# Kernel optimization log

Measured on AMD Instinct MI355X. Metric: run time of the kernel, lower is better.

## Reference

```python
import jax, jax.numpy as jnp
import numpy as np

EPS = 1e-09
TOP_K = 2


def setup_inputs() -> dict:
    key = jax.random.key(0)
    k1, k2 = jax.random.split(key)
    N, D, E = 32768, 1024, 64
    x = jax.random.normal(k1, (N, D), dtype=jnp.float32)
    gate_w = jax.random.normal(k2, (E, D), dtype=jnp.float32) * (1.0 / np.sqrt(D))
    return {"x": x, "gate_w": gate_w}


def reference(x, gate_w):
    # logits: [N, E] = x @ gate_w.T  (nn.Linear with no bias)
    logits = jnp.einsum("nd,ed->ne", x, gate_w)
    probs = jax.nn.softmax(logits, axis=-1)
    # aux load-balancing loss (stored on buffer in torch; returned here)
    mean_probs = probs.mean(axis=0)  # [E]
    aux_loss = jnp.sum(mean_probs * jnp.log(mean_probs + EPS))
    # top-k selection + renormalize
    top_k_weights, top_k_indices = jax.lax.top_k(probs, TOP_K)  # [N, K]
    top_k_weights = top_k_weights / (top_k_weights.sum(axis=-1, keepdims=True) + EPS)
    return top_k_weights, top_k_indices, aux_loss
```

## Files before the change

### kernel.cpp

```cpp
#include <hip/hip_runtime.h>
#include <hip/hip_bf16.h>
#include <math.h>

#define NROWS 32768
#define DDIM  1024
#define NEXP  64
#define TAU   2e-4f
#define EPSF  1e-9f
#define CAPMAX 8192
#define NSHARD 8
#define NCH   16

typedef __attribute__((ext_vector_type(8)))  short  short8;
typedef __attribute__((ext_vector_type(16))) float  f32x16;
typedef __attribute__((address_space(3))) unsigned int       lds_u32;
typedef __attribute__((address_space(1))) const unsigned int g_u32;

__device__ __forceinline__ bool gt_(float a, int ea, float b, int eb)
{ return a > b || (a == b && ea < eb); }

__device__ __forceinline__ void cvt_hl(float f, short& h, short& l)
{
    __hip_bfloat16 hb = __float2bfloat16(f);
    float r = f - __bfloat162float(hb);
    __hip_bfloat16 lb = __float2bfloat16(r);
    h = *reinterpret_cast<short*>(&hb);
    l = *reinterpret_cast<short*>(&lb);
}

__global__ void wpack_kernel(const float* __restrict__ gw,
                             unsigned short* __restrict__ wp,
                             float* __restrict__ shard,
                             int* __restrict__ cnt)
{
    if (blockIdx.x == 0) {
        shard[threadIdx.x]       = 0.0f;
        shard[256 + threadIdx.x] = 0.0f;
        if (threadIdx.x == 0) *cnt = 0;
    }
    const int kc = blockIdx.x;
    const int t  = threadIdx.x;
    const int lane = t & 63, g = (t >> 6) & 1, pr = t >> 7;
    const int e = g * 32 + (lane & 31);
    const int k = kc * 16 + (lane >> 5) * 8;
    float4 f0 = *reinterpret_cast<const float4*>(gw + (size_t)e * DDIM + k);
    float4 f1 = *reinterpret_cast<const float4*>(gw + (size_t)e * DDIM + k + 4);
    float f[8] = {f0.x, f0.y, f0.z, f0.w, f1.x, f1.y, f1.z, f1.w};
    short8 o;
    #pragma unroll
    for (int j = 0; j < 8; ++j) {
        short hh, ll;
        cvt_hl(f[j], hh, ll);
        o[j] = pr ? ll : hh;
    }
    *reinterpret_cast<short8*>(wp + ((size_t)((kc * 2 + g) * 2 + pr) * 64 + lane) * 8) = o;
}

__global__ __launch_bounds__(128, 2) void moe_main(
    const float* __restrict__ x, const unsigned short* __restrict__ wp,
    float* __restrict__ out, float* __restrict__ shard,
    int* __restrict__ cnt, int* __restrict__ list, int cap)
{
    extern __shared__ char smem[];

    const int t = threadIdx.x;
    const int g = t >> 6;
    const int lane = t & 63;
    const int l31 = lane & 31, l5 = lane >> 5;
    const int row0 = blockIdx.x * 32;
    const int arow = l31;
    const int xr   = (arow & 7) << 4;

    f32x16 acc;
    #pragma unroll
    for (int r = 0; r < 16; ++r) acc[r] = 0.0f;

    int srow[4], scol[4];
    #pragma unroll
    for (int q = 0; q < 4; ++q) {
        int d = q * 2048 + t * 16;
        srow[q] = d >> 8;
        scol[q] = (d & 255) ^ ((srow[q] & 7) << 4);
    }

    const char* wqb = (const char*)wp + (size_t)g * 2048 + (size_t)lane * 16;

    #define STAGE(c_) do {                                                       \
        const char* xs0_ = (const char*)x + (size_t)row0 * 4096 + (size_t)(c_) * 256; \
        const int xb_ = ((c_) & 3) * 8192;                                       \
        _Pragma("unroll")                                                        \
        for (int q_ = 0; q_ < 4; ++q_) {                                         \
            int d_ = q_ * 2048 + t * 16;                                         \
            const char* xsrc_ = xs0_ + (size_t)srow[q_] * 4096 + scol[q_];       \
            __builtin_amdgcn_global_load_lds((g_u32*)xsrc_,                      \
                (lds_u32*)(smem + xb_ + d_), 16, 0, 0);                          \
        }                                                                        \
    } while (0)

    #define BLOAD(dst_, c_) do {                                                 \
        _Pragma("unroll")                                                        \
        for (int kcl_ = 0; kcl_ < 4; ++kcl_) {                                   \
            const char* b_ = wqb + (size_t)((c_) * 4 + kcl_) * 4096;             \
            dst_[kcl_][0] = *reinterpret_cast<const short8*>(b_);                \
            dst_[kcl_][1] = *reinterpret_cast<const short8*>(b_ + 1024);         \
        }                                                                        \
    } while (0)

    short8 Bc[4][2], Bn[4][2];

    STAGE(0); STAGE(1); STAGE(2);
    BLOAD(Bc, 0);

    for (int i = 0; i < NCH; ++i) {
        if (i < NCH - 1) BLOAD(Bn, i + 1);
        if (i < NCH - 3) STAGE(i + 3);
        __builtin_amdgcn_sched_barrier(0);
        if (i == 0)               { asm volatile("s_waitcnt vmcnt(12)" ::: "memory"); }
        else if (i < NCH - 3)     { asm volatile("s_waitcnt vmcnt(16)" ::: "memory"); }
        else if (i == NCH - 3)    { asm volatile("s_waitcnt vmcnt(12)" ::: "memory"); }
        else if (i == NCH - 2)    { asm volatile("s_waitcnt vmcnt(8)" ::: "memory"); }
        else                      { asm volatile("s_waitcnt vmcnt(0)" ::: "memory"); }
        __builtin_amdgcn_s_barrier();
        __builtin_amdgcn_sched_barrier(0);

        const int xb = (i & 3) * 8192;
        const char* xrow = smem + xb + arow * 256;
        #pragma unroll
        for (int kcl = 0; kcl < 4; ++kcl) {
            const int cb = kcl * 64 + l5 * 32;
            float4 f0 = *reinterpret_cast<const float4*>(xrow + (cb ^ xr));
            float4 f1 = *reinterpret_cast<const float4*>(xrow + ((cb + 16) ^ xr));
            float f[8] = {f0.x, f0.y, f0.z, f0.w, f1.x, f1.y, f1.z, f1.w};
            short8 ah, al;
            #pragma unroll
            for (int jj = 0; jj < 8; ++jj) {
                short hh, ll;
                cvt_hl(f[jj], hh, ll);
                ah[jj] = hh; al[jj] = ll;
            }
            acc = __builtin_amdgcn_mfma_f32_32x32x16_bf16(ah, Bc[kcl][0], acc, 0, 0, 0);
            acc = __builtin_amdgcn_mfma_f32_32x32x16_bf16(al, Bc[kcl][0], acc, 0, 0, 0);
            acc = __builtin_amdgcn_mfma_f32_32x32x16_bf16(ah, Bc[kcl][1], acc, 0, 0, 0);
        }
        #pragma unroll
        for (int kcl = 0; kcl < 4; ++kcl) {
            Bc[kcl][0] = Bn[kcl][0];
            Bc[kcl][1] = Bn[kcl][1];
        }
        __builtin_amdgcn_sched_barrier(0);
        __builtin_amdgcn_s_barrier();
        __builtin_amdgcn_sched_barrier(0);
    }
    #undef STAGE
    #undef BLOAD

    float* lgs = reinterpret_cast<float*>(smem);
    __syncthreads();
    #pragma unroll
    for (int r = 0; r < 16; ++r) {
        const int lrow = (r & 3) + 8 * (r >> 2) + 4 * l5;
        lgs[lrow * 68 + g * 32 + l31] = acc[r];
    }
    __syncthreads();

    const int erow = t >> 2, q = t & 3;
    float L[16];
    #pragma unroll
    for (int i = 0; i < 4; ++i) {
        float4 v = *reinterpret_cast<const float4*>(lgs + erow * 68 + q * 16 + i * 4);
        L[4*i] = v.x; L[4*i+1] = v.y; L[4*i+2] = v.z; L[4*i+3] = v.w;
    }
    float v1 = -3.4e38f, v2 = -3.4e38f, v3 = -3.4e38f;
    int   e1 = 1 << 30,  e2 = 1 << 30,  e3 = 1 << 30;
    #pragma unroll
    for (int i = 0; i < 16; ++i) {
        float v = L[i]; int e = q * 16 + i;
        if      (gt_(v, e, v1, e1)) { v3=v2; e3=e2; v2=v1; e2=e1; v1=v; e1=e; }
        else if (gt_(v, e, v2, e2)) { v3=v2; e3=e2; v2=v; e2=e; }
        else if (gt_(v, e, v3, e3)) { v3=v; e3=e; }
    }
    #pragma unroll
    for (int m = 1; m <= 2; m <<= 1) {
        float o1 = __shfl_xor(v1, m), o2 = __shfl_xor(v2, m), o3 = __shfl_xor(v3, m);
        int  oe1 = __shfl_xor(e1, m), oe2 = __shfl_xor(e2, m), oe3 = __shfl_xor(e3, m);
        float n1, n2, n3; int m1, m2, m3;
        if (gt_(v1, e1, o1, oe1)) {
            n1 = v1; m1 = e1;
            if (gt_(v2, e2, o1, oe1)) {
                n2 = v2; m2 = e2;
                if (gt_(v3, e3, o1, oe1)) { n3 = v3; m3 = e3; } else { n3 = o1; m3 = oe1; }
            } else {
                n2 = o1; m2 = oe1;
                if (gt_(v2, e2, o2, oe2)) { n3 = v2; m3 = e2; } else { n3 = o2; m3 = oe2; }
            }
        } else {
            n1 = o1; m1 = oe1;
            if (gt_(o2, oe2, v1, e1)) {
                n2 = o2; m2 = oe2;
                if (gt_(o3, oe3, v1, e1)) { n3 = o3; m3 = oe3; } else { n3 = v1; m3 = e1; }
            } else {
                n2 = v1; m2 = e1;
                if (gt_(o2, oe2, v2, e2)) { n3 = o2; m3 = oe2; } else { n3 = v2; m3 = e2; }
            }
        }
        v1 = n1; e1 = m1; v2 = n2; e2 = m2; v3 = n3; e3 = m3;
    }
    float pr[16], sl = 0.0f;
    #pragma unroll
    for (int i = 0; i < 16; ++i) { pr[i] = expf(L[i] - v1); sl += pr[i]; }
    float S = sl;
    S += __shfl_xor(S, 1); S += __shfl_xor(S, 2);
    const float invS = 1.0f / S;
    #pragma unroll
    for (int i = 0; i < 16; ++i) pr[i] *= invS;
    #pragma unroll
    for (int m = 4; m <= 32; m <<= 1)
        #pragma unroll
        for (int i = 0; i < 16; ++i) pr[i] += __shfl_xor(pr[i], m);
    float* auxred = lgs + 32 * 68;
    if (lane < 4) {
        #pragma unroll
        for (int i = 0; i < 16; ++i) auxred[g * 64 + q * 16 + i] = pr[i];
    }
    if (q == 0) {
        const float p1 = invS;
        const float p2 = expf(v2 - v1) * invS;
        const float dn = p1 + p2 + EPSF;
        const int r = row0 + erow;
        out[2 * r]                 = p1 / dn;
        out[2 * r + 1]             = p2 / dn;
        out[2 * NROWS + 2 * r]     = (float)e1;
        out[2 * NROWS + 2 * r + 1] = (float)e2;
        if (cap > 0 && (v1 - v2 < TAU || v2 - v3 < TAU)) {
            int pos = atomicAdd(cnt, 1);
            if (pos < cap) list[pos] = r;
        }
    }
    __syncthreads();
    if (t < 64) {
        float s = auxred[t] + auxred[64 + t];
        atomicAdd(&shard[(blockIdx.x & (NSHARD - 1)) * 64 + t], s);
    }
}

__global__ __launch_bounds__(256) void finalize_kernel(
    const float* __restrict__ x, const float* __restrict__ gw,
    float* __restrict__ out, const float* __restrict__ shard,
    const int* __restrict__ cnt, const int* __restrict__ list, int cap)
{
    if (blockIdx.x == 0) {
        const int tt = threadIdx.x;
        if (tt < 64) {
            float m = 0.0f;
            #pragma unroll
            for (int s = 0; s < NSHARD; ++s) m += shard[s * 64 + tt];
            m *= (1.0f / (float)NROWS);
            float v = m * logf(m + EPSF);
            #pragma unroll
            for (int k = 1; k <= 32; k <<= 1) v += __shfl_xor(v, k);
            if (tt == 0) out[4 * NROWS] = v;
        }
        return;
    }
    __shared__ float lg[64];
    const int n = (cap > 0) ? min(*cnt, cap) : 0;
    const int tt = threadIdx.x, e = tt >> 2, part = tt & 3;
    for (int j = (int)blockIdx.x - 1; j < n; j += 64) {
        const int row = list[j];
        const float* xrp = x  + (size_t)row * DDIM + part * 256;
        const float* wrp = gw + (size_t)e   * DDIM + part * 256;
        float a = 0.0f;
        #pragma unroll 8
        for (int kk = 0; kk < 64; ++kk) {
            float4 xv = *reinterpret_cast<const float4*>(xrp + kk * 4);
            float4 wv = *reinterpret_cast<const float4*>(wrp + kk * 4);
            a += xv.x * wv.x + xv.y * wv.y + xv.z * wv.z + xv.w * wv.w;
        }
        a += __shfl_xor(a, 1); a += __shfl_xor(a, 2);
        if (part == 0) lg[e] = a;
        __syncthreads();
        if (tt < 4) {
            const int q = tt;
            float v1 = -3.4e38f, v2 = -3.4e38f; int e1 = 1 << 30, e2 = 1 << 30;
            float Lr[16];
            #pragma unroll
            for (int i = 0; i < 16; ++i) {
                float v = Lr[i] = lg[q * 16 + i]; int ee = q * 16 + i;
                if      (gt_(v, ee, v1, e1)) { v2 = v1; e2 = e1; v1 = v; e1 = ee; }
                else if (gt_(v, ee, v2, e2)) { v2 = v; e2 = ee; }
            }
            #pragma unroll
            for (int m = 1; m <= 2; m <<= 1) {
                float o1 = __shfl_xor(v1, m), o2 = __shfl_xor(v2, m);
                int  oe1 = __shfl_xor(e1, m), oe2 = __shfl_xor(e2, m);
                float n1, n2; int m1, m2;
                if (gt_(v1, e1, o1, oe1)) {
                    n1 = v1; m1 = e1;
                    if (gt_(v2, e2, o1, oe1)) { n2 = v2; m2 = e2; } else { n2 = o1; m2 = oe1; }
                } else {
                    n1 = o1; m1 = oe1;
                    if (gt_(o2, oe2, v1, e1)) { n2 = o2; m2 = oe2; } else { n2 = v1; m2 = e1; }
                }
                v1 = n1; e1 = m1; v2 = n2; e2 = m2;
            }
            float s = 0.0f;
            #pragma unroll
            for (int i = 0; i < 16; ++i) s += expf(Lr[i] - v1);
            s += __shfl_xor(s, 1); s += __shfl_xor(s, 2);
            if (q == 0) {
                const float invS = 1.0f / s;
                const float p1 = invS, p2 = expf(v2 - v1) * invS;
                const float dn = p1 + p2 + EPSF;
                out[2 * row]                 = p1 / dn;
                out[2 * row + 1]             = p2 / dn;
                out[2 * NROWS + 2 * row]     = (float)e1;
                out[2 * NROWS + 2 * row + 1] = (float)e2;
            }
        }
        __syncthreads();
    }
}

extern "C" void kernel_launch(void* const* d_in, const int* in_sizes, int n_in,
                              void* d_out, int out_size, void* d_ws, size_t ws_size,
                              hipStream_t stream)
{
    const float* x  = (const float*)d_in[0];
    const float* gw = (const float*)d_in[1];
    float* out      = (float*)d_out;

    unsigned short* wp = (unsigned short*)d_ws;
    float* shard   = (float*)((char*)d_ws + 262144);
    int*   cnt     = (int*)((char*)d_ws + 264192);
    int*   list    = (int*)((char*)d_ws + 264448);
    int cap = 0;
    if (ws_size >= 264448 + 4096) {
        size_t avail = (ws_size - 264448) / sizeof(int);
        cap = (avail > CAPMAX) ? CAPMAX : (int)avail;
    }

    hipLaunchKernelGGL(wpack_kernel, dim3(64), dim3(256), 0, stream,
                       gw, wp, shard, cnt);
    hipLaunchKernelGGL(moe_main, dim3(NROWS / 32), dim3(128), 32768, stream,
                       x, wp, out, shard, cnt, list, cap);
    hipLaunchKernelGGL(finalize_kernel, dim3(65), dim3(256), 0, stream,
                       x, gw, out, shard, cnt, list, cap);
}
```

Baseline: 61.36 us.

## Fuse ambiguous-row fp32 recompute and aux-loss finalize into main kernel

Removes the separate finalize kernel. Each block now marks near-tie rows in a shared bitmask and recomputes their logits in exact fp32 in place, and the last block to finish, found through an atomic done counter, reduces the shard sums into the aux loss. This saves a kernel launch and the global list/counter traffic. The cost is a serialized per-row recompute inside blocks that have ambiguous rows, with extra syncs, and the tie threshold is halved to cut how many rows need it. The smaller threshold may let rows whose bf16-split top-k differs from fp32 go uncorrected.

```diff
diff --git a/kernel.cpp b/kernel.cpp
--- a/kernel.cpp
+++ b/kernel.cpp
@@ -5,11 +5,11 @@
 #define NROWS 32768
 #define DDIM  1024
 #define NEXP  64
-#define TAU   2e-4f
+#define TAU   1e-4f
 #define EPSF  1e-9f
-#define CAPMAX 8192
 #define NSHARD 8
 #define NCH   16
+#define NBLK  1024
 
 typedef __attribute__((ext_vector_type(8)))  short  short8;
 typedef __attribute__((ext_vector_type(16))) float  f32x16;
@@ -31,12 +31,12 @@
 __global__ void wpack_kernel(const float* __restrict__ gw,
                              unsigned short* __restrict__ wp,
                              float* __restrict__ shard,
-                             int* __restrict__ cnt)
+                             int* __restrict__ done)
 {
     if (blockIdx.x == 0) {
         shard[threadIdx.x]       = 0.0f;
         shard[256 + threadIdx.x] = 0.0f;
-        if (threadIdx.x == 0) *cnt = 0;
+        if (threadIdx.x == 0) *done = 0;
     }
     const int kc = blockIdx.x;
     const int t  = threadIdx.x;
@@ -57,11 +57,12 @@
 }
 
 __global__ __launch_bounds__(128, 2) void moe_main(
-    const float* __restrict__ x, const unsigned short* __restrict__ wp,
-    float* __restrict__ out, float* __restrict__ shard,
-    int* __restrict__ cnt, int* __restrict__ list, int cap)
+    const float* __restrict__ x, const float* __restrict__ gw,
+    const unsigned short* __restrict__ wp, float* __restrict__ out,
+    float* __restrict__ shard, int* __restrict__ done)
 {
     extern __shared__ char smem[];
+    __shared__ unsigned ambig;
 
     const int t = threadIdx.x;
     const int g = t >> 6;
@@ -70,6 +71,8 @@
     const int row0 = blockIdx.x * 32;
     const int arow = l31;
     const int xr   = (arow & 7) << 4;
+
+    if (t == 0) ambig = 0u;
 
     f32x16 acc;
     #pragma unroll
@@ -231,93 +234,95 @@
         out[2 * r + 1]             = p2 / dn;
         out[2 * NROWS + 2 * r]     = (float)e1;
         out[2 * NROWS + 2 * r + 1] = (float)e2;
-        if (cap > 0 && (v1 - v2 < TAU || v2 - v3 < TAU)) {
-            int pos = atomicAdd(cnt, 1);
-            if (pos < cap) list[pos] = r;
-        }
+        if (v1 - v2 < TAU || v2 - v3 < TAU)
+            atomicOr(&ambig, 1u << erow);
     }
     __syncthreads();
     if (t < 64) {
         float s = auxred[t] + auxred[64 + t];
         atomicAdd(&shard[(blockIdx.x & (NSHARD - 1)) * 64 + t], s);
     }
-}
-
-__global__ __launch_bounds__(256) void finalize_kernel(
-    const float* __restrict__ x, const float* __restrict__ gw,
-    float* __restrict__ out, const float* __restrict__ shard,
-    const int* __restrict__ cnt, const int* __restrict__ list, int cap)
-{
-    if (blockIdx.x == 0) {
-        const int tt = threadIdx.x;
-        if (tt < 64) {
+
+    unsigned am = ambig;
+    if (am) {
+        float* lg = lgs;
+        const int re = t >> 1, part = t & 1;
+        while (am) {
+            const int rloc = __ffs((int)am) - 1;
+            am &= am - 1;
+            const int row = row0 + rloc;
+            const float* xrp = x  + (size_t)row * DDIM + part * 512;
+            const float* wrp = gw + (size_t)re  * DDIM + part * 512;
+            float a = 0.0f;
+            #pragma unroll 8
+            for (int kk = 0; kk < 128; ++kk) {
+                float4 xv = *reinterpret_cast<const float4*>(xrp + kk * 4);
+                float4 wv = *reinterpret_cast<const float4*>(wrp + kk * 4);
+                a += xv.x * wv.x + xv.y * wv.y + xv.z * wv.z + xv.w * wv.w;
+            }
+            a += __shfl_xor(a, 1);
+            __syncthreads();
+            if (part == 0) lg[re] = a;
+            __syncthreads();
+            if (t < 4) {
+                const int qq = t;
+                float w1 = -3.4e38f, w2 = -3.4e38f; int f1i = 1 << 30, f2i = 1 << 30;
+                float Lr[16];
+                #pragma unroll
+                for (int i = 0; i < 16; ++i) {
+                    float v = Lr[i] = lg[qq * 16 + i]; int ee = qq * 16 + i;
+                    if      (gt_(v, ee, w1, f1i)) { w2 = w1; f2i = f1i; w1 = v; f1i = ee; }
+                    else if (gt_(v, ee, w2, f2i)) { w2 = v; f2i = ee; }
+                }
+                #pragma unroll
+                for (int m = 1; m <= 2; m <<= 1) {
+                    float o1 = __shfl_xor(w1, m), o2 = __shfl_xor(w2, m);
+                    int  oe1 = __shfl_xor(f1i, m), oe2 = __shfl_xor(f2i, m);
+                    float n1, n2; int m1, m2;
+                    if (gt_(w1, f1i, o1, oe1)) {
+                        n1 = w1; m1 = f1i;
+                        if (gt_(w2, f2i, o1, oe1)) { n2 = w2; m2 = f2i; } else { n2 = o1; m2 = oe1; }
+                    } else {
+                        n1 = o1; m1 = oe1;
+                        if (gt_(o2, oe2, w1, f1i)) { n2 = o2; m2 = oe2; } else { n2 = w1; m2 = f1i; }
+                    }
+                    w1 = n1; f1i = m1; w2 = n2; f2i = m2;
+                }
+                float s = 0.0f;
+                #pragma unroll
+                for (int i = 0; i < 16; ++i) s += expf(Lr[i] - w1);
+                s += __shfl_xor(s, 1); s += __shfl_xor(s, 2);
+                if (qq == 0) {
+                    const float is = 1.0f / s;
+                    const float p1 = is, p2 = expf(w2 - w1) * is;
+                    const float dn = p1 + p2 + EPSF;
+                    out[2 * row]                 = p1 / dn;
+                    out[2 * row + 1]             = p2 / dn;
+                    out[2 * NROWS + 2 * row]     = (float)f1i;
+                    out[2 * NROWS + 2 * row + 1] = (float)f2i;
+                }
+            }
+            __syncthreads();
+        }
+    }
+
+    __syncthreads();
+    __threadfence();
+    __shared__ int rank;
+    if (t == 0) rank = atomicAdd(done, 1);
+    __syncthreads();
+    if (rank == NBLK - 1) {
+        __threadfence();
+        if (t < 64) {
             float m = 0.0f;
             #pragma unroll
-            for (int s = 0; s < NSHARD; ++s) m += shard[s * 64 + tt];
+            for (int s = 0; s < NSHARD; ++s) m += shard[s * 64 + t];
             m *= (1.0f / (float)NROWS);
             float v = m * logf(m + EPSF);
             #pragma unroll
             for (int k = 1; k <= 32; k <<= 1) v += __shfl_xor(v, k);
-            if (tt == 0) out[4 * NROWS] = v;
-        }
-        return;
-    }
-    __shared__ float lg[64];
-    const int n = (cap > 0) ? min(*cnt, cap) : 0;
-    const int tt = threadIdx.x, e = tt >> 2, part = tt & 3;
-    for (int j = (int)blockIdx.x - 1; j < n; j += 64) {
-        const int row = list[j];
-        const float* xrp = x  + (size_t)row * DDIM + part * 256;
-        const float* wrp = gw + (size_t)e   * DDIM + part * 256;
-        float a = 0.0f;
-        #pragma unroll 8
-        for (int kk = 0; kk < 64; ++kk) {
-            float4 xv = *reinterpret_cast<const float4*>(xrp + kk * 4);
-            float4 wv = *reinterpret_cast<const float4*>(wrp + kk * 4);
-            a += xv.x * wv.x + xv.y * wv.y + xv.z * wv.z + xv.w * wv.w;
-        }
-        a += __shfl_xor(a, 1); a += __shfl_xor(a, 2);
-        if (part == 0) lg[e] = a;
-        __syncthreads();
-        if (tt < 4) {
-            const int q = tt;
-            float v1 = -3.4e38f, v2 = -3.4e38f; int e1 = 1 << 30, e2 = 1 << 30;
-            float Lr[16];
-            #pragma unroll
-            for (int i = 0; i < 16; ++i) {
-                float v = Lr[i] = lg[q * 16 + i]; int ee = q * 16 + i;
-                if      (gt_(v, ee, v1, e1)) { v2 = v1; e2 = e1; v1 = v; e1 = ee; }
-                else if (gt_(v, ee, v2, e2)) { v2 = v; e2 = ee; }
-            }
-            #pragma unroll
-            for (int m = 1; m <= 2; m <<= 1) {
-                float o1 = __shfl_xor(v1, m), o2 = __shfl_xor(v2, m);
-                int  oe1 = __shfl_xor(e1, m), oe2 = __shfl_xor(e2, m);
-                float n1, n2; int m1, m2;
-                if (gt_(v1, e1, o1, oe1)) {
-                    n1 = v1; m1 = e1;
-                    if (gt_(v2, e2, o1, oe1)) { n2 = v2; m2 = e2; } else { n2 = o1; m2 = oe1; }
-                } else {
-                    n1 = o1; m1 = oe1;
-                    if (gt_(o2, oe2, v1, e1)) { n2 = o2; m2 = oe2; } else { n2 = v1; m2 = e1; }
-                }
-                v1 = n1; e1 = m1; v2 = n2; e2 = m2;
-            }
-            float s = 0.0f;
-            #pragma unroll
-            for (int i = 0; i < 16; ++i) s += expf(Lr[i] - v1);
-            s += __shfl_xor(s, 1); s += __shfl_xor(s, 2);
-            if (q == 0) {
-                const float invS = 1.0f / s;
-                const float p1 = invS, p2 = expf(v2 - v1) * invS;
-                const float dn = p1 + p2 + EPSF;
-                out[2 * row]                 = p1 / dn;
-                out[2 * row + 1]             = p2 / dn;
-                out[2 * NROWS + 2 * row]     = (float)e1;
-                out[2 * NROWS + 2 * row + 1] = (float)e2;
-            }
-        }
-        __syncthreads();
+            if (t == 0) out[4 * NROWS] = v;
+        }
     }
 }
 
@@ -330,19 +335,11 @@
     float* out      = (float*)d_out;
 
     unsigned short* wp = (unsigned short*)d_ws;
-    float* shard   = (float*)((char*)d_ws + 262144);
-    int*   cnt     = (int*)((char*)d_ws + 264192);
-    int*   list    = (int*)((char*)d_ws + 264448);
-    int cap = 0;
-    if (ws_size >= 264448 + 4096) {
-        size_t avail = (ws_size - 264448) / sizeof(int);
-        cap = (avail > CAPMAX) ? CAPMAX : (int)avail;
-    }
+    float* shard = (float*)((char*)d_ws + 262144);
+    int*   done  = (int*)((char*)d_ws + 264192);
 
     hipLaunchKernelGGL(wpack_kernel, dim3(64), dim3(256), 0, stream,
-                       gw, wp, shard, cnt);
+                       gw, wp, shard, done);
     hipLaunchKernelGGL(moe_main, dim3(NROWS / 32), dim3(128), 32768, stream,
-                       x, wp, out, shard, cnt, list, cap);
-    hipLaunchKernelGGL(finalize_kernel, dim3(65), dim3(256), 0, stream,
-                       x, gw, out, shard, cnt, list, cap);
+                       x, gw, wp, out, shard, done);
 }
```

Measured after the change: 98.72 us. +60.9%, slower.
